# Optimization experiments

Measured on AMD Instinct MI355X. Metric: run time of the kernel, lower is better.

Reference implementation:

```python
import jax, jax.numpy as jnp
import numpy as np


def setup_inputs() -> dict:
    key = jax.random.key(0)
    k1, k2, k3 = jax.random.split(key, 3)
    B, H, S, D = 4, 16, 2048, 64
    queries = jax.random.normal(k1, (B, H, S, D), dtype=jnp.float32)
    keys = jax.random.normal(k2, (B, H, S, D), dtype=jnp.float32)
    values = jax.random.normal(k3, (B, H, S, D), dtype=jnp.float32)
    return {"queries": queries, "keys": keys, "values": values, "d_k": D}


def reference(queries, keys, values, d_k):
    # scores = Q K^T / sqrt(d_k)  -> [B, H, S, S]
    scale = 1.0 / jnp.sqrt(jnp.asarray(d_k, dtype=queries.dtype))
    scores = jnp.einsum("bhqd,bhkd->bhqk", queries, keys) * scale
    weights = jax.nn.softmax(scores, axis=-1)
    # out = weights V -> [B, H, S, D]
    return jnp.einsum("bhqk,bhkd->bhqd", weights, values)
```

## Files before the change

kernel.cpp:

```cpp
#include <hip/hip_runtime.h>
#include <hip/hip_bf16.h>

typedef __attribute__((ext_vector_type(8))) short short8;
typedef __attribute__((ext_vector_type(4))) short short4v;
typedef __attribute__((ext_vector_type(16))) float f32x16;

constexpr int Sn = 2048, Dn = 64;
constexpr int KVB = 64;
constexpr int QB  = 256;
constexpr int NT  = Sn / KVB;
constexpr int KSTR = 72;
constexpr int VSTR = 68;
constexpr float QSC = 0.18033688011112042f;
constexpr float DTH = 8.0f;

struct SMemS { short K[2][KVB][KSTR]; short Vt[2][Dn][VSTR]; };
union  SMem  { SMemS s; float ep[4][32][36]; };

__device__ inline unsigned cvt_pk_bf16(float a, float b) {
  unsigned r;
  asm("v_cvt_pk_bf16_f32 %0, %1, %2" : "=v"(r) : "v"(a), "v"(b));
  return r;
}
__device__ inline short8 catw(unsigned a, unsigned b, unsigned c, unsigned d) {
  union { unsigned u[4]; short8 s; } t;
  t.u[0]=a; t.u[1]=b; t.u[2]=c; t.u[3]=d;
  return t.s;
}
__device__ inline short8 pack8(float4 a, float4 b) {
  return catw(cvt_pk_bf16(a.x,a.y), cvt_pk_bf16(a.z,a.w),
              cvt_pk_bf16(b.x,b.y), cvt_pk_bf16(b.z,b.w));
}
__device__ inline short8 cat4(short4v a, short4v b) {
  short8 r;
  r[0]=a[0]; r[1]=a[1]; r[2]=a[2]; r[3]=a[3];
  r[4]=b[0]; r[5]=b[1]; r[6]=b[2]; r[7]=b[3];
  return r;
}

__global__ __launch_bounds__(256, 2)
void attn_fwd(const float* __restrict__ Qm, const float* __restrict__ Km,
              const float* __restrict__ Vm, float* __restrict__ Om) {
  __shared__ alignas(16) SMem sm;

  const int fid = blockIdx.x + (blockIdx.y << 3);
  const int xcd = fid & 7, w = fid >> 3;
  const int qt = w & 7, bh = (xcd << 3) | (w >> 3);

  const size_t base = (size_t)bh * Sn * Dn;
  const float* Qb = Qm + base;
  const float* Kb = Km + base;
  const float* Vb = Vm + base;
  float*       Ob = Om + base;

  const int tid = threadIdx.x, wv = tid >> 6, lane = tid & 63;
  const int il = lane & 31, hi = lane >> 5;
  const int qr0 = qt * QB + wv * 64;

  short8 qf[2][4];
#pragma unroll
  for (int u = 0; u < 2; ++u)
#pragma unroll
    for (int ks = 0; ks < 4; ++ks) {
      const float4* qp = (const float4*)(Qb + (size_t)(qr0 + u*32 + il) * Dn + ks*16 + hi*8);
      float4 a = qp[0], b = qp[1];
      a.x*=QSC; a.y*=QSC; a.z*=QSC; a.w*=QSC;
      b.x*=QSC; b.y*=QSC; b.z*=QSC; b.w*=QSC;
      qf[u][ks] = pack8(a, b);
    }

  f32x16 acc[2][2];
#pragma unroll
  for (int u = 0; u < 2; ++u)
#pragma unroll
    for (int dt = 0; dt < 2; ++dt)
#pragma unroll
      for (int r = 0; r < 16; ++r) acc[u][dt][r] = 0.f;
  float m_run[2] = {-1e30f, -1e30f}, l_run[2] = {0.f, 0.f};

  const int krow = tid >> 2, kc = (tid & 3) * 16;
  const int vd = tid & 63, vk0 = (tid >> 6) * 8;

  auto stageK = [&](int buf, float4 a0, float4 a1, float4 a2, float4 a3) {
    *(short8*)&sm.s.K[buf][krow][kc]     = pack8(a0, a1);
    *(short8*)&sm.s.K[buf][krow][kc + 8] = pack8(a2, a3);
  };
  auto stageV = [&](int buf, const float* vv) {
#pragma unroll
    for (int c = 0; c < 2; ++c) {
      union { unsigned u[2]; short4v s; } t0, t1;
      t0.u[0] = cvt_pk_bf16(vv[c*8+0], vv[c*8+1]);
      t0.u[1] = cvt_pk_bf16(vv[c*8+2], vv[c*8+3]);
      t1.u[0] = cvt_pk_bf16(vv[c*8+4], vv[c*8+5]);
      t1.u[1] = cvt_pk_bf16(vv[c*8+6], vv[c*8+7]);
      short* p = &sm.s.Vt[buf][vd][vk0 + c*32];
      *(short4v*)p       = t0.s;
      *(short4v*)(p + 4) = t1.s;
    }
  };

  {
    const float4* kp = (const float4*)(Kb + (size_t)krow * Dn + kc);
    float4 a0 = kp[0], a1 = kp[1], a2 = kp[2], a3 = kp[3];
    float vv[16];
#pragma unroll
    for (int c = 0; c < 2; ++c)
#pragma unroll
      for (int j = 0; j < 8; ++j) vv[c*8+j] = Vb[(size_t)(vk0 + c*32 + j) * Dn + vd];
    stageK(0, a0, a1, a2, a3);
    stageV(0, vv);
  }
  __syncthreads();

  int cur = 0;
  for (int t = 0; t < NT; ++t) {
    const bool pf = (t + 1 < NT);
    float4 na0, na1, na2, na3; float nv[16];
    if (pf) {
      const int kvn = (t + 1) * KVB;
      const float4* kp = (const float4*)(Kb + (size_t)(kvn + krow) * Dn + kc);
      na0 = kp[0]; na1 = kp[1]; na2 = kp[2]; na3 = kp[3];
#pragma unroll
      for (int c = 0; c < 2; ++c)
#pragma unroll
        for (int j = 0; j < 8; ++j) nv[c*8+j] = Vb[(size_t)(kvn + vk0 + c*32 + j) * Dn + vd];
    }

    short8 kf[2][4];
#pragma unroll
    for (int h = 0; h < 2; ++h)
#pragma unroll
      for (int ks = 0; ks < 4; ++ks)
        kf[h][ks] = *(const short8*)&sm.s.K[cur][h*32 + il][ks*16 + hi*8];

    short8 pb[2][2][2];
#pragma unroll
    for (int u = 0; u < 2; ++u) {
      f32x16 sa[2];
#pragma unroll
      for (int h = 0; h < 2; ++h) {
#pragma unroll
        for (int r = 0; r < 16; ++r) sa[h][r] = 0.f;
#pragma unroll
        for (int ks = 0; ks < 4; ++ks)
          sa[h] = __builtin_amdgcn_mfma_f32_32x32x16_bf16(kf[h][ks], qf[u][ks], sa[h], 0, 0, 0);
      }
      float mx = sa[0][0];
#pragma unroll
      for (int h = 0; h < 2; ++h)
#pragma unroll
        for (int r = 0; r < 16; ++r) mx = fmaxf(mx, sa[h][r]);
      mx = fmaxf(mx, __shfl_xor(mx, 32));
      if (__any(mx > m_run[u] + DTH)) {
        float mnew = fmaxf(m_run[u], mx);
        float corr = __builtin_amdgcn_exp2f(m_run[u] - mnew);
        l_run[u] *= corr;
#pragma unroll
        for (int dt = 0; dt < 2; ++dt)
#pragma unroll
          for (int r = 0; r < 16; ++r) acc[u][dt][r] *= corr;
        m_run[u] = mnew;
      }
      const float m0 = m_run[u];
      float ls = 0.f;
#pragma unroll
      for (int h = 0; h < 2; ++h)
#pragma unroll
        for (int r = 0; r < 16; ++r) {
          float p = __builtin_amdgcn_exp2f(sa[h][r] - m0);
          sa[h][r] = p; ls += p;
        }
      ls += __shfl_xor(ls, 32);
      l_run[u] += ls;
#pragma unroll
      for (int h = 0; h < 2; ++h) {
        pb[u][h][0] = catw(cvt_pk_bf16(sa[h][0],  sa[h][1]),  cvt_pk_bf16(sa[h][2],  sa[h][3]),
                           cvt_pk_bf16(sa[h][4],  sa[h][5]),  cvt_pk_bf16(sa[h][6],  sa[h][7]));
        pb[u][h][1] = catw(cvt_pk_bf16(sa[h][8],  sa[h][9]),  cvt_pk_bf16(sa[h][10], sa[h][11]),
                           cvt_pk_bf16(sa[h][12], sa[h][13]), cvt_pk_bf16(sa[h][14], sa[h][15]));
      }
    }

    if (pf) { stageK(cur ^ 1, na0, na1, na2, na3); stageV(cur ^ 1, nv); }

#pragma unroll
    for (int h = 0; h < 2; ++h)
#pragma unroll
      for (int dt = 0; dt < 2; ++dt) {
        const short* vrow = &sm.s.Vt[cur][dt*32 + il][h*32];
        short8 va = cat4(*(const short4v*)(vrow + 4*hi),      *(const short4v*)(vrow + 8  + 4*hi));
        short8 vb = cat4(*(const short4v*)(vrow + 16 + 4*hi), *(const short4v*)(vrow + 24 + 4*hi));
#pragma unroll
        for (int u = 0; u < 2; ++u) {
          acc[u][dt] = __builtin_amdgcn_mfma_f32_32x32x16_bf16(va, pb[u][h][0], acc[u][dt], 0, 0, 0);
          acc[u][dt] = __builtin_amdgcn_mfma_f32_32x32x16_bf16(vb, pb[u][h][1], acc[u][dt], 0, 0, 0);
        }
      }
    __syncthreads();
    cur ^= 1;
  }

  const int q2 = lane >> 1, dh = (lane & 1) * 16;
#pragma unroll
  for (int u = 0; u < 2; ++u) {
    const float inv = 1.0f / l_run[u];
#pragma unroll
    for (int dt = 0; dt < 2; ++dt) {
#pragma unroll
      for (int r = 0; r < 16; ++r) {
        int dcol = (r & 3) + 8 * (r >> 2) + 4 * hi;
        sm.ep[wv][il][dcol] = acc[u][dt][r] * inv;
      }
#pragma unroll
      for (int i = 0; i < 4; ++i) {
        float4 o = *(const float4*)&sm.ep[wv][q2][dh + i*4];
        *(float4*)(Ob + (size_t)(qr0 + u*32 + q2) * Dn + dt*32 + dh + i*4) = o;
      }
    }
  }
}

extern "C" void kernel_launch(void* const* d_in, const int* in_sizes, int n_in,
                              void* d_out, int out_size, void* d_ws, size_t ws_size,
                              hipStream_t stream) {
  const float* Q = (const float*)d_in[0];
  const float* K = (const float*)d_in[1];
  const float* V = (const float*)d_in[2];
  float* O = (float*)d_out;
  dim3 grid(Sn / QB, 4 * 16);
  attn_fwd<<<grid, 256, 0, stream>>>(Q, K, V, O);
}
```

Before: 99.52 us.

## Halve query tile per block to one 32-row subtile per wave, raise occupancy

Shrinks the query block from 256 to 128 rows so each wave handles a single 32-row query subtile instead of two. This doubles the grid and raises the launch-bounds occupancy hint from 2 to 4 blocks per CU, aiming to cut register pressure and hide latency. The row max and row sum now use a tree reduction instead of a serial chain. In exchange, every K/V tile is staged to LDS twice as often per query row, which doubles global K/V traffic and conversion work, and the K fragments are no longer reused across two query subtiles.

```diff
diff --git a/kernel.cpp b/kernel.cpp
--- a/kernel.cpp
+++ b/kernel.cpp
@@ -7,7 +7,7 @@
 
 constexpr int Sn = 2048, Dn = 64;
 constexpr int KVB = 64;
-constexpr int QB  = 256;
+constexpr int QB  = 128;
 constexpr int NT  = Sn / KVB;
 constexpr int KSTR = 72;
 constexpr int VSTR = 68;
@@ -38,14 +38,14 @@
   return r;
 }
 
-__global__ __launch_bounds__(256, 2)
+__global__ __launch_bounds__(256, 4)
 void attn_fwd(const float* __restrict__ Qm, const float* __restrict__ Km,
               const float* __restrict__ Vm, float* __restrict__ Om) {
   __shared__ alignas(16) SMem sm;
 
-  const int fid = blockIdx.x + (blockIdx.y << 3);
+  const int fid = blockIdx.x + (blockIdx.y << 4);
   const int xcd = fid & 7, w = fid >> 3;
-  const int qt = w & 7, bh = (xcd << 3) | (w >> 3);
+  const int qt = w & 15, bh = (xcd << 3) | (w >> 4);
 
   const size_t base = (size_t)bh * Sn * Dn;
   const float* Qb = Qm + base;
@@ -55,28 +55,22 @@
 
   const int tid = threadIdx.x, wv = tid >> 6, lane = tid & 63;
   const int il = lane & 31, hi = lane >> 5;
-  const int qr0 = qt * QB + wv * 64;
-
-  short8 qf[2][4];
-#pragma unroll
-  for (int u = 0; u < 2; ++u)
-#pragma unroll
-    for (int ks = 0; ks < 4; ++ks) {
-      const float4* qp = (const float4*)(Qb + (size_t)(qr0 + u*32 + il) * Dn + ks*16 + hi*8);
-      float4 a = qp[0], b = qp[1];
-      a.x*=QSC; a.y*=QSC; a.z*=QSC; a.w*=QSC;
-      b.x*=QSC; b.y*=QSC; b.z*=QSC; b.w*=QSC;
-      qf[u][ks] = pack8(a, b);
-    }
-
-  f32x16 acc[2][2];
-#pragma unroll
-  for (int u = 0; u < 2; ++u)
-#pragma unroll
-    for (int dt = 0; dt < 2; ++dt)
-#pragma unroll
-      for (int r = 0; r < 16; ++r) acc[u][dt][r] = 0.f;
-  float m_run[2] = {-1e30f, -1e30f}, l_run[2] = {0.f, 0.f};
+  const int qrow = qt * QB + wv * 32 + il;
+
+  short8 qf[4];
+#pragma unroll
+  for (int ks = 0; ks < 4; ++ks) {
+    const float4* qp = (const float4*)(Qb + (size_t)qrow * Dn + ks*16 + hi*8);
+    float4 a = qp[0], b = qp[1];
+    a.x*=QSC; a.y*=QSC; a.z*=QSC; a.w*=QSC;
+    b.x*=QSC; b.y*=QSC; b.z*=QSC; b.w*=QSC;
+    qf[ks] = pack8(a, b);
+  }
+
+  f32x16 acc[2];
+#pragma unroll
+  for (int r = 0; r < 16; ++r) { acc[0][r] = 0.f; acc[1][r] = 0.f; }
+  float m_run = -1e30f, l_run = 0.f;
 
   const int krow = tid >> 2, kc = (tid & 3) * 16;
   const int vd = tid & 63, vk0 = (tid >> 6) * 8;
@@ -126,59 +120,58 @@
         for (int j = 0; j < 8; ++j) nv[c*8+j] = Vb[(size_t)(kvn + vk0 + c*32 + j) * Dn + vd];
     }
 
-    short8 kf[2][4];
+    f32x16 sa[2];
+#pragma unroll
+    for (int h = 0; h < 2; ++h) {
+#pragma unroll
+      for (int r = 0; r < 16; ++r) sa[h][r] = 0.f;
+#pragma unroll
+      for (int ks = 0; ks < 4; ++ks) {
+        short8 kf = *(const short8*)&sm.s.K[cur][h*32 + il][ks*16 + hi*8];
+        sa[h] = __builtin_amdgcn_mfma_f32_32x32x16_bf16(kf, qf[ks], sa[h], 0, 0, 0);
+      }
+    }
+
+    float tm[16];
+#pragma unroll
+    for (int r = 0; r < 16; ++r) tm[r] = fmaxf(sa[0][r], sa[1][r]);
+#pragma unroll
+    for (int s = 8; s > 0; s >>= 1)
+#pragma unroll
+      for (int r = 0; r < s; ++r) tm[r] = fmaxf(tm[r], tm[r + s]);
+    float mx = fmaxf(tm[0], __shfl_xor(tm[0], 32));
+
+    if (__any(mx > m_run + DTH)) {
+      float mnew = fmaxf(m_run, mx);
+      float corr = __builtin_amdgcn_exp2f(m_run - mnew);
+      l_run *= corr;
+#pragma unroll
+      for (int dt = 0; dt < 2; ++dt)
+#pragma unroll
+        for (int r = 0; r < 16; ++r) acc[dt][r] *= corr;
+      m_run = mnew;
+    }
+    const float m0 = m_run;
 #pragma unroll
     for (int h = 0; h < 2; ++h)
 #pragma unroll
-      for (int ks = 0; ks < 4; ++ks)
-        kf[h][ks] = *(const short8*)&sm.s.K[cur][h*32 + il][ks*16 + hi*8];
-
-    short8 pb[2][2][2];
-#pragma unroll
-    for (int u = 0; u < 2; ++u) {
-      f32x16 sa[2];
-#pragma unroll
-      for (int h = 0; h < 2; ++h) {
-#pragma unroll
-        for (int r = 0; r < 16; ++r) sa[h][r] = 0.f;
-#pragma unroll
-        for (int ks = 0; ks < 4; ++ks)
-          sa[h] = __builtin_amdgcn_mfma_f32_32x32x16_bf16(kf[h][ks], qf[u][ks], sa[h], 0, 0, 0);
-      }
-      float mx = sa[0][0];
-#pragma unroll
-      for (int h = 0; h < 2; ++h)
-#pragma unroll
-        for (int r = 0; r < 16; ++r) mx = fmaxf(mx, sa[h][r]);
-      mx = fmaxf(mx, __shfl_xor(mx, 32));
-      if (__any(mx > m_run[u] + DTH)) {
-        float mnew = fmaxf(m_run[u], mx);
-        float corr = __builtin_amdgcn_exp2f(m_run[u] - mnew);
-        l_run[u] *= corr;
-#pragma unroll
-        for (int dt = 0; dt < 2; ++dt)
-#pragma unroll
-          for (int r = 0; r < 16; ++r) acc[u][dt][r] *= corr;
-        m_run[u] = mnew;
-      }
-      const float m0 = m_run[u];
-      float ls = 0.f;
-#pragma unroll
-      for (int h = 0; h < 2; ++h)
-#pragma unroll
-        for (int r = 0; r < 16; ++r) {
-          float p = __builtin_amdgcn_exp2f(sa[h][r] - m0);
-          sa[h][r] = p; ls += p;
-        }
-      ls += __shfl_xor(ls, 32);
-      l_run[u] += ls;
-#pragma unroll
-      for (int h = 0; h < 2; ++h) {
-        pb[u][h][0] = catw(cvt_pk_bf16(sa[h][0],  sa[h][1]),  cvt_pk_bf16(sa[h][2],  sa[h][3]),
-                           cvt_pk_bf16(sa[h][4],  sa[h][5]),  cvt_pk_bf16(sa[h][6],  sa[h][7]));
-        pb[u][h][1] = catw(cvt_pk_bf16(sa[h][8],  sa[h][9]),  cvt_pk_bf16(sa[h][10], sa[h][11]),
-                           cvt_pk_bf16(sa[h][12], sa[h][13]), cvt_pk_bf16(sa[h][14], sa[h][15]));
-      }
+      for (int r = 0; r < 16; ++r) sa[h][r] = __builtin_amdgcn_exp2f(sa[h][r] - m0);
+    float ta[16];
+#pragma unroll
+    for (int r = 0; r < 16; ++r) ta[r] = sa[0][r] + sa[1][r];
+#pragma unroll
+    for (int s = 8; s > 0; s >>= 1)
+#pragma unroll
+      for (int r = 0; r < s; ++r) ta[r] += ta[r + s];
+    l_run += ta[0] + __shfl_xor(ta[0], 32);
+
+    short8 pb[2][2];
+#pragma unroll
+    for (int h = 0; h < 2; ++h) {
+      pb[h][0] = catw(cvt_pk_bf16(sa[h][0],  sa[h][1]),  cvt_pk_bf16(sa[h][2],  sa[h][3]),
+                      cvt_pk_bf16(sa[h][4],  sa[h][5]),  cvt_pk_bf16(sa[h][6],  sa[h][7]));
+      pb[h][1] = catw(cvt_pk_bf16(sa[h][8],  sa[h][9]),  cvt_pk_bf16(sa[h][10], sa[h][11]),
+                      cvt_pk_bf16(sa[h][12], sa[h][13]), cvt_pk_bf16(sa[h][14], sa[h][15]));
     }
 
     if (pf) { stageK(cur ^ 1, na0, na1, na2, na3); stageV(cur ^ 1, nv); }
@@ -190,32 +183,26 @@
         const short* vrow = &sm.s.Vt[cur][dt*32 + il][h*32];
         short8 va = cat4(*(const short4v*)(vrow + 4*hi),      *(const short4v*)(vrow + 8  + 4*hi));
         short8 vb = cat4(*(const short4v*)(vrow + 16 + 4*hi), *(const short4v*)(vrow + 24 + 4*hi));
-#pragma unroll
-        for (int u = 0; u < 2; ++u) {
-          acc[u][dt] = __builtin_amdgcn_mfma_f32_32x32x16_bf16(va, pb[u][h][0], acc[u][dt], 0, 0, 0);
-          acc[u][dt] = __builtin_amdgcn_mfma_f32_32x32x16_bf16(vb, pb[u][h][1], acc[u][dt], 0, 0, 0);
-        }
+        acc[dt] = __builtin_amdgcn_mfma_f32_32x32x16_bf16(va, pb[h][0], acc[dt], 0, 0, 0);
+        acc[dt] = __builtin_amdgcn_mfma_f32_32x32x16_bf16(vb, pb[h][1], acc[dt], 0, 0, 0);
       }
     __syncthreads();
     cur ^= 1;
   }
 
+  const float inv = 1.0f / l_run;
   const int q2 = lane >> 1, dh = (lane & 1) * 16;
 #pragma unroll
-  for (int u = 0; u < 2; ++u) {
-    const float inv = 1.0f / l_run[u];
-#pragma unroll
-    for (int dt = 0; dt < 2; ++dt) {
-#pragma unroll
-      for (int r = 0; r < 16; ++r) {
-        int dcol = (r & 3) + 8 * (r >> 2) + 4 * hi;
-        sm.ep[wv][il][dcol] = acc[u][dt][r] * inv;
-      }
-#pragma unroll
-      for (int i = 0; i < 4; ++i) {
-        float4 o = *(const float4*)&sm.ep[wv][q2][dh + i*4];
-        *(float4*)(Ob + (size_t)(qr0 + u*32 + q2) * Dn + dt*32 + dh + i*4) = o;
-      }
+  for (int dt = 0; dt < 2; ++dt) {
+#pragma unroll
+    for (int r = 0; r < 16; ++r) {
+      int dcol = (r & 3) + 8 * (r >> 2) + 4 * hi;
+      sm.ep[wv][il][dcol] = acc[dt][r] * inv;
+    }
+#pragma unroll
+    for (int i = 0; i < 4; ++i) {
+      float4 o = *(const float4*)&sm.ep[wv][q2][dh + i*4];
+      *(float4*)(Ob + (size_t)(qt * QB + wv * 32 + q2) * Dn + dt*32 + dh + i*4) = o;
     }
   }
 }
```

After: 133.3 us. 1.34x slower.

## Batch QK MFMAs for both query halves, tree-reduce softmax, raise MFMA priority

Applied to the files above, without the earlier changes.

Issues all QK^T MFMAs for both 32-row query groups up front, using a shared zero accumulator, instead of interleaving them with each group's softmax. The serial max and sum chains become tree reductions to shorten dependency latency. Both MFMA phases are wrapped in s_setprio so waves doing matrix work get issue priority over waves doing softmax. Keeping all four score tiles live adds 32 VGPRs of accumulator state, which could hurt occupancy at the 2-waves-per-SIMD launch bound.

```diff
diff --git a/kernel.cpp b/kernel.cpp
--- a/kernel.cpp
+++ b/kernel.cpp
@@ -77,6 +77,10 @@
 #pragma unroll
       for (int r = 0; r < 16; ++r) acc[u][dt][r] = 0.f;
   float m_run[2] = {-1e30f, -1e30f}, l_run[2] = {0.f, 0.f};
+
+  f32x16 fz;
+#pragma unroll
+  for (int r = 0; r < 16; ++r) fz[r] = 0.f;
 
   const int krow = tid >> 2, kc = (tid & 3) * 16;
   const int vd = tid & 63, vk0 = (tid >> 6) * 8;
@@ -133,24 +137,31 @@
       for (int ks = 0; ks < 4; ++ks)
         kf[h][ks] = *(const short8*)&sm.s.K[cur][h*32 + il][ks*16 + hi*8];
 
+    f32x16 sa[2][2];
+    __builtin_amdgcn_s_setprio(1);
+#pragma unroll
+    for (int u = 0; u < 2; ++u)
+#pragma unroll
+      for (int h = 0; h < 2; ++h) {
+        sa[u][h] = __builtin_amdgcn_mfma_f32_32x32x16_bf16(kf[h][0], qf[u][0], fz, 0, 0, 0);
+#pragma unroll
+        for (int ks = 1; ks < 4; ++ks)
+          sa[u][h] = __builtin_amdgcn_mfma_f32_32x32x16_bf16(kf[h][ks], qf[u][ks], sa[u][h], 0, 0, 0);
+      }
+    __builtin_amdgcn_s_setprio(0);
+
     short8 pb[2][2][2];
 #pragma unroll
     for (int u = 0; u < 2; ++u) {
-      f32x16 sa[2];
-#pragma unroll
-      for (int h = 0; h < 2; ++h) {
-#pragma unroll
-        for (int r = 0; r < 16; ++r) sa[h][r] = 0.f;
-#pragma unroll
-        for (int ks = 0; ks < 4; ++ks)
-          sa[h] = __builtin_amdgcn_mfma_f32_32x32x16_bf16(kf[h][ks], qf[u][ks], sa[h], 0, 0, 0);
-      }
-      float mx = sa[0][0];
-#pragma unroll
-      for (int h = 0; h < 2; ++h)
-#pragma unroll
-        for (int r = 0; r < 16; ++r) mx = fmaxf(mx, sa[h][r]);
-      mx = fmaxf(mx, __shfl_xor(mx, 32));
+      float tm[16];
+#pragma unroll
+      for (int r = 0; r < 16; ++r) tm[r] = fmaxf(sa[u][0][r], sa[u][1][r]);
+#pragma unroll
+      for (int s = 8; s > 0; s >>= 1)
+#pragma unroll
+        for (int r = 0; r < s; ++r) tm[r] = fmaxf(tm[r], tm[r + s]);
+      float mx = fmaxf(tm[0], __shfl_xor(tm[0], 32));
+
       if (__any(mx > m_run[u] + DTH)) {
         float mnew = fmaxf(m_run[u], mx);
         float corr = __builtin_amdgcn_exp2f(m_run[u] - mnew);
@@ -162,27 +173,31 @@
         m_run[u] = mnew;
       }
       const float m0 = m_run[u];
-      float ls = 0.f;
 #pragma unroll
       for (int h = 0; h < 2; ++h)
 #pragma unroll
-        for (int r = 0; r < 16; ++r) {
-          float p = __builtin_amdgcn_exp2f(sa[h][r] - m0);
-          sa[h][r] = p; ls += p;
-        }
-      ls += __shfl_xor(ls, 32);
-      l_run[u] += ls;
+        for (int r = 0; r < 16; ++r) sa[u][h][r] = __builtin_amdgcn_exp2f(sa[u][h][r] - m0);
+      float ta[16];
+#pragma unroll
+      for (int r = 0; r < 16; ++r) ta[r] = sa[u][0][r] + sa[u][1][r];
+#pragma unroll
+      for (int s = 8; s > 0; s >>= 1)
+#pragma unroll
+        for (int r = 0; r < s; ++r) ta[r] += ta[r + s];
+      l_run[u] += ta[0] + __shfl_xor(ta[0], 32);
+
 #pragma unroll
       for (int h = 0; h < 2; ++h) {
-        pb[u][h][0] = catw(cvt_pk_bf16(sa[h][0],  sa[h][1]),  cvt_pk_bf16(sa[h][2],  sa[h][3]),
-                           cvt_pk_bf16(sa[h][4],  sa[h][5]),  cvt_pk_bf16(sa[h][6],  sa[h][7]));
-        pb[u][h][1] = catw(cvt_pk_bf16(sa[h][8],  sa[h][9]),  cvt_pk_bf16(sa[h][10], sa[h][11]),
-                           cvt_pk_bf16(sa[h][12], sa[h][13]), cvt_pk_bf16(sa[h][14], sa[h][15]));
+        pb[u][h][0] = catw(cvt_pk_bf16(sa[u][h][0],  sa[u][h][1]),  cvt_pk_bf16(sa[u][h][2],  sa[u][h][3]),
+                           cvt_pk_bf16(sa[u][h][4],  sa[u][h][5]),  cvt_pk_bf16(sa[u][h][6],  sa[u][h][7]));
+        pb[u][h][1] = catw(cvt_pk_bf16(sa[u][h][8],  sa[u][h][9]),  cvt_pk_bf16(sa[u][h][10], sa[u][h][11]),
+                           cvt_pk_bf16(sa[u][h][12], sa[u][h][13]), cvt_pk_bf16(sa[u][h][14], sa[u][h][15]));
       }
     }
 
     if (pf) { stageK(cur ^ 1, na0, na1, na2, na3); stageV(cur ^ 1, nv); }
 
+    __builtin_amdgcn_s_setprio(1);
 #pragma unroll
     for (int h = 0; h < 2; ++h)
 #pragma unroll
@@ -196,6 +211,7 @@
           acc[u][dt] = __builtin_amdgcn_mfma_f32_32x32x16_bf16(vb, pb[u][h][1], acc[u][dt], 0, 0, 0);
         }
       }
+    __builtin_amdgcn_s_setprio(0);
     __syncthreads();
     cur ^= 1;
   }
```

After: 101.8 us. +2.2%, slower.
